# Kernel tuning notes

Measured on AMD Instinct MI355X. Metric: run time of the kernel, lower is better.

The kernel has to match this reference:

```python
import jax, jax.numpy as jnp
import numpy as np

K_NN = 3  # knn(feat_y, feat_x, 3, ...) in the original

def setup_inputs() -> dict:
    key = jax.random.key(0)
    k1, k2, k3, k4, k5, k6 = jax.random.split(key, 6)
    B, C, H, W = 2, 64, 112, 112
    S, G = 50, 120
    img1_feature = jax.random.normal(k1, (B, C, H, W), dtype=jnp.float32)
    img2_feature = jax.random.normal(k2, (B, C, H, W), dtype=jnp.float32)
    mask1 = jax.random.randint(k3, (B, H, W), 0, 2).astype(bool)
    mask2 = jax.random.randint(k4, (B, H, W), 0, 2).astype(bool)
    src_pixel_group = jax.random.uniform(k5, (B, S, G, 2), dtype=jnp.float32)
    slic = jax.random.randint(k6, (B, H, W), 0, 50).astype(jnp.int32)
    return {"img1_feature": img1_feature, "img2_feature": img2_feature,
            "mask1": mask1, "mask2": mask2,
            "src_pixel_group": src_pixel_group, "slic": slic}

def _form_pred_corr(img1_feature, img2_feature, mask1, mask2):
    B, C, H, W = img1_feature.shape
    N = H * W
    fx = img1_feature.reshape(B, C, N)  # src features  [B,C,N]
    fy = img2_feature.reshape(B, C, N)  # dst features  [B,C,N]
    # cosine-KNN search (no_grad in the original): mask invalid dst pixels
    fxn = fx / (jnp.linalg.norm(fx, axis=1, keepdims=True) + 1e-12)
    fyn = fy / (jnp.linalg.norm(fy, axis=1, keepdims=True) + 1e-12)
    sims = jnp.einsum('bcn,bcm->bnm', fxn, fyn)  # [B,N,M] cosine sim
    sims = jnp.where(mask2.reshape(B, 1, N), sims, -jnp.inf)
    _, idx = jax.lax.top_k(jax.lax.stop_gradient(sims), K_NN)  # [B,N,K]
    # gather raw dst features at the K matched pixels: [B,N,K,C]
    fyT = fy.transpose(0, 2, 1)  # [B,M,C]
    gath = jax.vmap(lambda f, i: f[i])(fyT, idx.reshape(B, -1)).reshape(B, N, K_NN, C)
    # weights = raw dot product feat_x . feat_y (matches sim_xy in source)
    w = jnp.einsum('bnkc,bnc->bnk', gath, fx.transpose(0, 2, 1))  # [B,N,K]
    hh = (idx // W).astype(w.dtype)  # dst row coords
    ww = (idx % W).astype(w.dtype)   # dst col coords
    den = jnp.sum(w, axis=2)  # [B,N]
    num = jnp.stack([jnp.sum(hh * w, axis=2), jnp.sum(ww * w, axis=2)], axis=-1)
    pred = num / den[..., None]  # weighted-average dst position [B,N,2]
    pred_corr = jnp.where(mask1[..., None], pred.reshape(B, H, W, 2), -1.0)
    return pred_corr

def _slic_gather(pred_corr, src_pixel_group, norm_h):
    B, H, W, _ = pred_corr.shape
    S, G = src_pixel_group.shape[1], src_pixel_group.shape[2]
    # round(src * H), clamp to [0, H-1] (256/255 in the original at H=256)
    pix = jnp.clip(jnp.round(src_pixel_group * H).astype(jnp.int32), 0, H - 1)
    lin = pix[..., 0] * W + pix[..., 1]  # [B,S,G]
    pcf = pred_corr.reshape(B, H * W, 2)
    dst = jax.vmap(lambda p, l: p[l])(pcf, lin.reshape(B, S * G))
    return dst.reshape(B, S, G, 2) / norm_h

def reference(img1_feature, img2_feature, mask1, mask2, src_pixel_group, slic):
    pred_corr = _form_pred_corr(img1_feature, img2_feature, mask1, mask2)
    dst_pixel_group = _slic_gather(pred_corr, src_pixel_group, slic.shape[1])
    return pred_corr, dst_pixel_group
```

## Files before the change

kernel.cpp:

```cpp
#include <hip/hip_runtime.h>
#include <math.h>

typedef _Float16 f16;
typedef f16 f16x8 __attribute__((ext_vector_type(8)));
typedef float f32x16 __attribute__((ext_vector_type(16)));
typedef unsigned short u16;
typedef unsigned int u32;
typedef unsigned long long u64;
typedef u32 u32x4 __attribute__((ext_vector_type(4)));

#define B_ 2
#define C_ 64
#define KS 5
#define H_ 112
#define W_ 112
#define N_ 12544
#define S_ 50
#define G_ 120
#define SPLIT 8
#define LCAP 4
#define CPR (SPLIT*2*LCAP)
#define TMAX 400
#define CMAPN 12800
#define CH 13

#define NEGINF (-__builtin_inff())
#define FMED3 __builtin_amdgcn_fmed3f

union U16B { uint4 u; f16x8 h; f16 e[8]; };


__global__ void detect_fmt(const u32* __restrict__ m1, const u32* __restrict__ m2,
                           int nw, int* __restrict__ hdr) {
    __shared__ u32 s[2];
    if (threadIdx.x == 0) { s[0] = 0; s[1] = 0; }
    __syncthreads();
    u32 a = 0, bb = 0;
    for (int i = threadIdx.x; i < nw; i += blockDim.x) {
        a  |= m1[i] & 0xFFFFFF00u;
        bb |= m2[i] & 0xFFFFFF00u;
    }
    if (a)  atomicOr(&s[0], 1u);
    if (bb) atomicOr(&s[1], 1u);
    __syncthreads();
    if (threadIdx.x == 0) { hdr[0] = s[0] ? 1 : 0; hdr[1] = s[1] ? 1 : 0; }
}

__global__ __launch_bounds__(1024)
void scan_compact(const unsigned char* __restrict__ m1,
                  const unsigned char* __restrict__ m2,
                  int* __restrict__ hdr,
                  int* __restrict__ slotX, int* __restrict__ slotY,
                  int* __restrict__ cmapX, int* __restrict__ cmapY) {
    const int side = blockIdx.x >> 1;
    const int b = blockIdx.x & 1;
    const unsigned char* mk = side ? m2 : m1;
    const int flag = hdr[side];
    int* slotmap = side ? slotY : slotX;
    int* cmap    = side ? cmapY : cmapX;
    const int cntidx = side ? (2 + b) : (4 + b);

    __shared__ int ssum[1024];
    const int tid = threadIdx.x;
    const int m0 = tid * CH;

    u32 vbits = 0; int cnt = 0;
    #pragma unroll
    for (int i = 0; i < CH; ++i) {
        int m = m0 + i;
        int v = 0;
        if (m < N_) {
            int t = b * N_ + m;
            v = flag ? (mk[t] != 0) : (((const int*)mk)[t] != 0);
        }
        vbits |= (u32)v << i;
        cnt += v;
    }
    ssum[tid] = cnt;
    __syncthreads();
    #pragma unroll
    for (int d = 1; d < 1024; d <<= 1) {
        int v = (tid >= d) ? ssum[tid - d] : 0;
        __syncthreads();
        ssum[tid] += v;
        __syncthreads();
    }
    int slot = ssum[tid] - cnt;
    #pragma unroll
    for (int i = 0; i < CH; ++i) {
        int m = m0 + i;
        if (m < N_) {
            int t = b * N_ + m;
            if ((vbits >> i) & 1) {
                slotmap[t] = slot;
                cmap[b * CMAPN + slot] = m;
                slot++;
            } else slotmap[t] = -1;
        }
    }
    if (tid == 1023) hdr[cntidx] = ssum[1023];
}

__global__ void prep(const float* __restrict__ fx, const float* __restrict__ fy,
                     const unsigned char* __restrict__ mask2b,
                     const int* __restrict__ hdr,
                     const int* __restrict__ slotX, const int* __restrict__ slotY,
                     f16* __restrict__ fxq, float* __restrict__ fxT,
                     float* __restrict__ fynT, f16* __restrict__ fynq,
                     float* __restrict__ nyeps, float* __restrict__ minf,
                     float* __restrict__ out) {
    int t = blockIdx.x * blockDim.x + threadIdx.x;
    if (t >= B_ * N_) return;
    int b = t / N_;

    if (blockIdx.y == 0) {
        const float* src = fx + (size_t)b * C_ * N_ + (t - b * N_);
        float v[64];
        #pragma unroll
        for (int c = 0; c < C_; ++c) v[c] = src[(size_t)c * N_];

        float4* xT = (float4*)(fxT + (size_t)t * C_);
        #pragma unroll
        for (int c4 = 0; c4 < 16; ++c4)
            xT[c4] = make_float4(v[c4*4], v[c4*4+1], v[c4*4+2], v[c4*4+3]);

        int slot = slotX[t];
        if (slot < 0) {
            out[2 * (size_t)t] = -1.0f;
            out[2 * (size_t)t + 1] = -1.0f;
            return;
        }
        int tile = slot >> 5, r = slot & 31;
        uint4* q4 = (uint4*)fxq;
        size_t cb = (size_t)(b * TMAX + tile) * (KS * 64);
        #pragma unroll
        for (int ks = 0; ks < KS; ++ks) {
            #pragma unroll
            for (int hi = 0; hi < 2; ++hi) {
                U16B tmp;
                #pragma unroll
                for (int i = 0; i < 8; ++i) {
                    int k = 16 * ks + 8 * hi + i;
                    float val = (k < 64) ? v[k] : ((k == 64) ? 1.0f : 0.0f);
                    tmp.e[i] = (f16)val;
                }
                q4[cb + (size_t)ks * 64 + hi * 32 + r] = tmp.u;
            }
        }
    } else {
        const float* src = fy + (size_t)b * C_ * N_ + (t - b * N_);
        float v[64];
        float ss = 0.f;
        #pragma unroll
        for (int c = 0; c < C_; ++c) { v[c] = src[(size_t)c * N_]; ss = fmaf(v[c], v[c], ss); }
        float ny = sqrtf(ss) + 1e-12f;
        nyeps[t] = ny;
        int slot = slotY[t];
        minf[t] = (slot >= 0) ? 0.0f : NEGINF;

        float* dT = fynT + (size_t)t * C_;
        #pragma unroll
        for (int c = 0; c < C_; ++c) dT[c] = v[c] / ny;

        if (slot < 0) return;
        int tile = slot >> 5, r = slot & 31;
        uint4* q4 = (uint4*)fynq;
        size_t cb = (size_t)(b * TMAX + tile) * (KS * 64);
        #pragma unroll
        for (int ks = 0; ks < KS; ++ks) {
            #pragma unroll
            for (int hi = 0; hi < 2; ++hi) {
                U16B tmp;
                #pragma unroll
                for (int i = 0; i < 8; ++i) {
                    int k = 16 * ks + 8 * hi + i;
                    float val = (k < 64) ? (v[k] / ny) : ((k == 64) ? 128.0f : 0.0f);
                    tmp.e[i] = (f16)val;
                }
                q4[cb + (size_t)ks * 64 + hi * 32 + r] = tmp.u;
            }
        }
    }
}

__global__ void padfill(int* __restrict__ hdr, uint4* __restrict__ fynq4,
                        uint4* __restrict__ fxq4, int* __restrict__ cmapY,
                        int* __restrict__ cmapX) {
    int tid = threadIdx.x;
    __shared__ int sMY[2], sNX[2], sCY[2], sCX[2];
    if (tid == 0) {
        for (int b = 0; b < B_; ++b) {
            int cy = hdr[2 + b], cx = hdr[4 + b];
            int my = (cy + 255) & ~255;
            int nx = (cx + 63) & ~63;
            hdr[6 + b] = my; hdr[8 + b] = nx;
            sMY[b] = my; sNX[b] = nx; sCY[b] = cy; sCX[b] = cx;
        }
    }
    __syncthreads();
    uint4 z = make_uint4(0, 0, 0, 0);
    for (int b = 0; b < B_; ++b) {
        for (int p = sCY[b] + tid; p < sMY[b]; p += blockDim.x) {
            cmapY[b * CMAPN + p] = 0;
            int tile = p >> 5, r = p & 31;
            size_t cb = (size_t)(b * TMAX + tile) * (KS * 64);
            #pragma unroll
            for (int ks = 0; ks < KS; ++ks) {
                fynq4[cb + (size_t)ks * 64 + r] = z;
                fynq4[cb + (size_t)ks * 64 + 32 + r] = z;
            }
        }
        for (int p = sCX[b] + tid; p < sNX[b]; p += blockDim.x) {
            cmapX[b * CMAPN + p] = 0;
            int tile = p >> 5, r = p & 31;
            size_t cb = (size_t)(b * TMAX + tile) * (KS * 64);
            #pragma unroll
            for (int ks = 0; ks < KS; ++ks) {
                fxq4[cb + (size_t)ks * 64 + r] = z;
                fxq4[cb + (size_t)ks * 64 + 32 + r] = z;
            }
        }
    }
}

#define LDA(dst, t) { _Pragma("unroll") \
    for (int ks = 0; ks < KS; ++ks) \
        dst[ks] = fyb8[((size_t)(t) * KS + ks) * 64]; }

#define MFMAC(acc, a) { \
    acc = __builtin_amdgcn_mfma_f32_32x32x16_f16(a[0], bfr[0], zvec, 0, 0, 0); \
    acc = __builtin_amdgcn_mfma_f32_32x32x16_f16(a[1], bfr[1], acc, 0, 0, 0); \
    acc = __builtin_amdgcn_mfma_f32_32x32x16_f16(a[2], bfr[2], acc, 0, 0, 0); \
    acc = __builtin_amdgcn_mfma_f32_32x32x16_f16(a[3], bfr[3], acc, 0, 0, 0); \
    acc = __builtin_amdgcn_mfma_f32_32x32x16_f16(a[4], bfr[4], acc, 0, 0, 0); }

#define EXTRACT(acc, bse) { \
    _Pragma("unroll") \
    for (int r = 0; r < 16; ++r) { \
        u32 pb_ = (__float_as_uint(acc[r]) & VMASK) | ((bse) + (u32)r); \
        float p_ = __uint_as_float(pb_); \
        b4 = FMED3(p_, b3, b4); \
        b3 = FMED3(p_, b2, b3); \
        b2 = FMED3(p_, b1, b2); \
        b1 = fmaxf(p_, b1); } }

#define CELL(a, t) { f32x16 acc_; MFMAC(acc_, a); EXTRACT(acc_, (u32)((t) * 16)); }

__global__ __launch_bounds__(128, 4)
void stage1(const f16* __restrict__ fxq, const f16* __restrict__ fynq,
            const int* __restrict__ hdr,
            u32* __restrict__ cvals, u16* __restrict__ cidx) {
    const int tid = threadIdx.x;
    const int lane = tid & 63, w = tid >> 6;
    const int lo = lane & 31, hi = lane >> 5;
    const int gid = blockIdx.x;
    const int panel = gid & 15;
    const int b = panel >> 3, split = panel & 7;
    const int nt = (gid >> 4) * 2 + w;
    const int NXb = hdr[8 + b];
    if (nt * 32 >= NXb) return;
    const int TPSr = hdr[6 + b] >> 8;
    const int tbase = split * TPSr;

    const f16x8* fxq8 = (const f16x8*)fxq;
    const f16x8* fyb8 = (const f16x8*)fynq + ((size_t)(b * TMAX + tbase) * KS) * 64 + lane;

    u32 VMASK;
    asm("v_mov_b32 %0, 0xFFFFFC00" : "=v"(VMASK));

    f16x8 bfr[KS];
    #pragma unroll
    for (int ks = 0; ks < KS; ++ks)
        bfr[ks] = fxq8[((size_t)((b * TMAX + nt) * KS + ks)) * 64 + lane];

    f32x16 zvec = {};
    float b1 = 0.f, b2 = 0.f, b3 = 0.f, b4 = 0.f;

    f16x8 aA[KS], aB[KS];
    LDA(aA, 0);
    int t = 0;
    #pragma unroll 1
    for (; t + 1 < TPSr; t += 2) {
        LDA(aB, t + 1);
        CELL(aA, t);
        if (t + 2 < TPSr) LDA(aA, t + 2);
        CELL(aB, t + 1);
    }
    if (t < TPSr) CELL(aA, t);

    int n = nt * 32 + lo;
    size_t base = (((size_t)(b * N_ + n) * SPLIT + split) * 2 + hi) * LCAP;
    u32 pb0 = __float_as_uint(b1), pb1 = __float_as_uint(b2);
    u32 pb2 = __float_as_uint(b3), pb3 = __float_as_uint(b4);
    u32x4 pv = {pb0, pb1, pb2, pb3};
    u64 pidx = 0;
    u32 pbs[4] = {pb0, pb1, pb2, pb3};
    #pragma unroll
    for (int k = 0; k < 4; ++k) {
        int idx10 = (int)(pbs[k] & 1023u);
        int tl = idx10 >> 4, r = idx10 & 15;
        u32 mc = (u32)((tbase + tl) * 32 + (r & 3) + ((r >> 2) << 3) + (hi << 2));
        pidx |= (u64)(mc & 0xFFFFu) << (16 * k);
    }
    __builtin_nontemporal_store(pv, (u32x4*)&cvals[base]);
    __builtin_nontemporal_store(pidx, (u64*)&cidx[base]);
}

__global__ __launch_bounds__(256)
void rescore(const u32* __restrict__ cvals, const u16* __restrict__ cidx,
             const float* __restrict__ fxT, const float* __restrict__ fynT,
             const float* __restrict__ nyeps, const float* __restrict__ minf,
             const int* __restrict__ cmapX, const int* __restrict__ cmapY,
             const int* __restrict__ hdr, float* __restrict__ out) {
    int gwf = blockIdx.x * 4 + (threadIdx.x >> 6);
    int lane = threadIdx.x & 63;
    int b = gwf / N_, slot = gwf - b * N_;
    if (slot >= hdr[4 + b]) return;
    int orig_n = cmapX[b * CMAPN + slot];

    float vn = __uint_as_float(cvals[(size_t)(b * N_ + slot) * CPR + lane]);
    int cm = cidx[(size_t)(b * N_ + slot) * CPR + lane];

    float cur = vn;
    float t3 = NEGINF;
    #pragma unroll
    for (int r = 0; r < 3; ++r) {
        float c = cur;
        #pragma unroll
        for (int off = 32; off >= 1; off >>= 1) c = fmaxf(c, __shfl_xor(c, off));
        t3 = c;
        cur = (cur == c) ? NEGINF : cur;
    }
    bool redo = (vn >= t3 - 0.125f);

    float rnk = NEGINF, wgt = 0.f;
    int midx = 0x7fffffff;
    if (redo) {
        int om = cmapY[b * CMAPN + cm];
        const float4* xq4 = (const float4*)(fxT + ((size_t)b * N_ + orig_n) * C_);
        const float4* fr4 = (const float4*)(fynT + ((size_t)b * N_ + om) * C_);
        float a = 0.f;
        #pragma unroll
        for (int c4 = 0; c4 < 16; ++c4) {
            float4 xf = xq4[c4];
            float4 f  = fr4[c4];
            a = fmaf(xf.x, f.x, a);
            a = fmaf(xf.y, f.y, a);
            a = fmaf(xf.z, f.z, a);
            a = fmaf(xf.w, f.w, a);
        }
        rnk = a + minf[(size_t)b * N_ + om];
        wgt = a * nyeps[(size_t)b * N_ + om];
        midx = om;
    }

    int wi[3]; float ww[3];
    #pragma unroll
    for (int r = 0; r < 3; ++r) {
        float cv = rnk; int ci = midx; float cw = wgt;
        #pragma unroll
        for (int off = 32; off >= 1; off >>= 1) {
            float ov = __shfl_xor(cv, off);
            int   oi = __shfl_xor(ci, off);
            float ow = __shfl_xor(cw, off);
            bool take = (ov > cv) || (ov == cv && oi < ci);
            cv = take ? ov : cv; ci = take ? oi : ci; cw = take ? ow : cw;
        }
        wi[r] = ci; ww[r] = cw;
        if (midx == ci) rnk = NEGINF;
    }

    if (lane == 0) {
        float w0 = ww[0], w1 = ww[1], w2 = ww[2];
        float h0 = (float)(wi[0] / W_), h1 = (float)(wi[1] / W_), h2 = (float)(wi[2] / W_);
        float q0 = (float)(wi[0] % W_), q1 = (float)(wi[1] % W_), q2 = (float)(wi[2] % W_);
        float den = w0 + w1 + w2;
        float ph = (h0 * w0 + h1 * w1 + h2 * w2) / den;
        float pw = (q0 * w0 + q1 * w1 + q2 * w2) / den;
        out[2 * ((size_t)b * N_ + orig_n)]     = ph;
        out[2 * ((size_t)b * N_ + orig_n) + 1] = pw;
    }
}

__global__ void slic_gather(const float* __restrict__ spg,
                            const float* __restrict__ pred,
                            float* __restrict__ outg) {
    int t = blockIdx.x * blockDim.x + threadIdx.x;
    if (t >= B_ * S_ * G_) return;
    int b = t / (S_ * G_);
    float vh = spg[2 * t], vw = spg[2 * t + 1];
    int ph = (int)rintf(vh * (float)H_);
    int pw = (int)rintf(vw * (float)H_);
    ph = ph < 0 ? 0 : (ph > H_ - 1 ? H_ - 1 : ph);
    pw = pw < 0 ? 0 : (pw > H_ - 1 ? H_ - 1 : pw);
    int lin = ph * W_ + pw;
    outg[2 * t]     = pred[((size_t)b * N_ + lin) * 2]     / (float)H_;
    outg[2 * t + 1] = pred[((size_t)b * N_ + lin) * 2 + 1] / (float)H_;
}

extern "C" void kernel_launch(void* const* d_in, const int* in_sizes, int n_in,
                              void* d_out, int out_size, void* d_ws, size_t ws_size,
                              hipStream_t stream) {
    const float* img1 = (const float*)d_in[0];
    const float* img2 = (const float*)d_in[1];
    const void*  mask1 = d_in[2];
    const void*  mask2 = d_in[3];
    const float* spg = (const float*)d_in[4];
    float* out = (float*)d_out;

    char* ws = (char*)d_ws;
    size_t off = 0;
    int*   hdr   = (int*)(ws + off);            off += 256;
    float* fynT  = (float*)(ws + off);          off += (size_t)B_ * N_ * C_ * 4;
    float* fxT   = (float*)(ws + off);          off += (size_t)B_ * N_ * C_ * 4;
    f16*   fxq   = (f16*)(ws + off);            off += (size_t)B_ * TMAX * KS * 64 * 16;
    f16*   fynq  = (f16*)(ws + off);            off += (size_t)B_ * TMAX * KS * 64 * 16;
    float* nyeps = (float*)(ws + off);          off += (size_t)B_ * N_ * 4;
    float* minf  = (float*)(ws + off);          off += (size_t)B_ * N_ * 4;
    int*   cmapY = (int*)(ws + off);            off += (size_t)B_ * CMAPN * 4;
    int*   cmapX = (int*)(ws + off);            off += (size_t)B_ * CMAPN * 4;
    int*   slotX = (int*)(ws + off);            off += (size_t)B_ * N_ * 4;
    int*   slotY = (int*)(ws + off);            off += (size_t)B_ * N_ * 4;
    u32*   cvals = (u32*)(ws + off);            off += (size_t)B_ * N_ * CPR * 4;
    u16*   cidx  = (u16*)(ws + off);            off += (size_t)B_ * N_ * CPR * 2;

    detect_fmt<<<1, 1024, 0, stream>>>((const u32*)mask1, (const u32*)mask2,
                                       (B_ * N_) / 4, hdr);
    scan_compact<<<4, 1024, 0, stream>>>((const unsigned char*)mask1,
                                         (const unsigned char*)mask2, hdr,
                                         slotX, slotY, cmapX, cmapY);
    dim3 gp((B_ * N_) / 256, 2);
    prep<<<gp, 256, 0, stream>>>(img1, img2, (const unsigned char*)mask2, hdr,
                                 slotX, slotY, fxq, fxT, fynT, fynq,
                                 nyeps, minf, out);
    padfill<<<1, 512, 0, stream>>>(hdr, (uint4*)fynq, (uint4*)fxq, cmapY, cmapX);

    stage1<<<3200, 128, 0, stream>>>(fxq, fynq, hdr, cvals, cidx);

    rescore<<<(B_ * N_) / 4, 256, 0, stream>>>(
        cvals, cidx, fxT, fynT, nyeps, minf, cmapX, cmapY, hdr, out);

    slic_gather<<<(B_ * S_ * G_ + 255) / 256, 256, 0, stream>>>(
        spg, out, out + (size_t)B_ * N_ * 2);
}
```

Measured before the change: 92.80 us.

## Fold mask format detection into scan and replace padfill with upfront zerofill

Removes the single-block detect_fmt kernel by having each scan_compact block detect the mask byte format itself, and replaces the serial single-block padfill with a wide grid-stride zerofill launched first. stage1 now computes padded counts from hdr directly. prep caches normalized dst features to avoid recomputing divisions. The aim is to cut small serial kernels from the critical path, at the cost of zeroing the full quantized buffers each call instead of only the pad region.

```diff
diff --git a/kernel.cpp b/kernel.cpp
--- a/kernel.cpp
+++ b/kernel.cpp
@@ -30,20 +30,15 @@
 union U16B { uint4 u; f16x8 h; f16 e[8]; };
 
 
-__global__ void detect_fmt(const u32* __restrict__ m1, const u32* __restrict__ m2,
-                           int nw, int* __restrict__ hdr) {
-    __shared__ u32 s[2];
-    if (threadIdx.x == 0) { s[0] = 0; s[1] = 0; }
-    __syncthreads();
-    u32 a = 0, bb = 0;
-    for (int i = threadIdx.x; i < nw; i += blockDim.x) {
-        a  |= m1[i] & 0xFFFFFF00u;
-        bb |= m2[i] & 0xFFFFFF00u;
-    }
-    if (a)  atomicOr(&s[0], 1u);
-    if (bb) atomicOr(&s[1], 1u);
-    __syncthreads();
-    if (threadIdx.x == 0) { hdr[0] = s[0] ? 1 : 0; hdr[1] = s[1] ? 1 : 0; }
+__global__ void zerofill(uint4* __restrict__ fxq4, uint4* __restrict__ fynq4,
+                         int* __restrict__ cmapX, int* __restrict__ cmapY) {
+    int i = blockIdx.x * blockDim.x + threadIdx.x;
+    int stride = gridDim.x * blockDim.x;
+    uint4 z = make_uint4(0, 0, 0, 0);
+    const int NQ = B_ * TMAX * KS * 64;
+    for (int k = i; k < NQ; k += stride) { fxq4[k] = z; fynq4[k] = z; }
+    const int NC = B_ * CMAPN;
+    for (int k = i; k < NC; k += stride) { cmapX[k] = 0; cmapY[k] = 0; }
 }
 
 __global__ __launch_bounds__(1024)
@@ -55,15 +50,23 @@
     const int side = blockIdx.x >> 1;
     const int b = blockIdx.x & 1;
     const unsigned char* mk = side ? m2 : m1;
-    const int flag = hdr[side];
     int* slotmap = side ? slotY : slotX;
     int* cmap    = side ? cmapY : cmapX;
     const int cntidx = side ? (2 + b) : (4 + b);
-
+    const int tid = threadIdx.x;
+
+    __shared__ int sflag;
     __shared__ int ssum[1024];
-    const int tid = threadIdx.x;
+    if (tid == 0) sflag = 0;
+    __syncthreads();
+    const u32* mw = (const u32*)mk;
+    u32 acc = 0;
+    for (int i = tid; i < (B_ * N_) / 4; i += 1024) acc |= mw[i] & 0xFFFFFF00u;
+    if (acc) atomicOr(&sflag, 1);
+    __syncthreads();
+    const int flag = sflag;
+
     const int m0 = tid * CH;
-
     u32 vbits = 0; int cnt = 0;
     #pragma unroll
     for (int i = 0; i < CH; ++i) {
@@ -102,8 +105,6 @@
 }
 
 __global__ void prep(const float* __restrict__ fx, const float* __restrict__ fy,
-                     const unsigned char* __restrict__ mask2b,
-                     const int* __restrict__ hdr,
                      const int* __restrict__ slotX, const int* __restrict__ slotY,
                      f16* __restrict__ fxq, float* __restrict__ fxT,
                      float* __restrict__ fynT, f16* __restrict__ fynq,
@@ -149,7 +150,7 @@
         }
     } else {
         const float* src = fy + (size_t)b * C_ * N_ + (t - b * N_);
-        float v[64];
+        float v[64], dv[64];
         float ss = 0.f;
         #pragma unroll
         for (int c = 0; c < C_; ++c) { v[c] = src[(size_t)c * N_]; ss = fmaf(v[c], v[c], ss); }
@@ -160,7 +161,7 @@
 
         float* dT = fynT + (size_t)t * C_;
         #pragma unroll
-        for (int c = 0; c < C_; ++c) dT[c] = v[c] / ny;
+        for (int c = 0; c < C_; ++c) { dv[c] = v[c] / ny; dT[c] = dv[c]; }
 
         if (slot < 0) return;
         int tile = slot >> 5, r = slot & 31;
@@ -174,50 +175,10 @@
                 #pragma unroll
                 for (int i = 0; i < 8; ++i) {
                     int k = 16 * ks + 8 * hi + i;
-                    float val = (k < 64) ? (v[k] / ny) : ((k == 64) ? 128.0f : 0.0f);
+                    float val = (k < 64) ? dv[k] : ((k == 64) ? 128.0f : 0.0f);
                     tmp.e[i] = (f16)val;
                 }
                 q4[cb + (size_t)ks * 64 + hi * 32 + r] = tmp.u;
-            }
-        }
-    }
-}
-
-__global__ void padfill(int* __restrict__ hdr, uint4* __restrict__ fynq4,
-                        uint4* __restrict__ fxq4, int* __restrict__ cmapY,
-                        int* __restrict__ cmapX) {
-    int tid = threadIdx.x;
-    __shared__ int sMY[2], sNX[2], sCY[2], sCX[2];
-    if (tid == 0) {
-        for (int b = 0; b < B_; ++b) {
-            int cy = hdr[2 + b], cx = hdr[4 + b];
-            int my = (cy + 255) & ~255;
-            int nx = (cx + 63) & ~63;
-            hdr[6 + b] = my; hdr[8 + b] = nx;
-            sMY[b] = my; sNX[b] = nx; sCY[b] = cy; sCX[b] = cx;
-        }
-    }
-    __syncthreads();
-    uint4 z = make_uint4(0, 0, 0, 0);
-    for (int b = 0; b < B_; ++b) {
-        for (int p = sCY[b] + tid; p < sMY[b]; p += blockDim.x) {
-            cmapY[b * CMAPN + p] = 0;
-            int tile = p >> 5, r = p & 31;
-            size_t cb = (size_t)(b * TMAX + tile) * (KS * 64);
-            #pragma unroll
-            for (int ks = 0; ks < KS; ++ks) {
-                fynq4[cb + (size_t)ks * 64 + r] = z;
-                fynq4[cb + (size_t)ks * 64 + 32 + r] = z;
-            }
-        }
-        for (int p = sCX[b] + tid; p < sNX[b]; p += blockDim.x) {
-            cmapX[b * CMAPN + p] = 0;
-            int tile = p >> 5, r = p & 31;
-            size_t cb = (size_t)(b * TMAX + tile) * (KS * 64);
-            #pragma unroll
-            for (int ks = 0; ks < KS; ++ks) {
-                fxq4[cb + (size_t)ks * 64 + r] = z;
-                fxq4[cb + (size_t)ks * 64 + 32 + r] = z;
             }
         }
     }
@@ -257,9 +218,9 @@
     const int panel = gid & 15;
     const int b = panel >> 3, split = panel & 7;
     const int nt = (gid >> 4) * 2 + w;
-    const int NXb = hdr[8 + b];
+    const int NXb = (hdr[4 + b] + 63) & ~63;
     if (nt * 32 >= NXb) return;
-    const int TPSr = hdr[6 + b] >> 8;
+    const int TPSr = ((hdr[2 + b] + 255) & ~255) >> 8;
     const int tbase = split * TPSr;
 
     const f16x8* fxq8 = (const f16x8*)fxq;
@@ -424,16 +385,13 @@
     u32*   cvals = (u32*)(ws + off);            off += (size_t)B_ * N_ * CPR * 4;
     u16*   cidx  = (u16*)(ws + off);            off += (size_t)B_ * N_ * CPR * 2;
 
-    detect_fmt<<<1, 1024, 0, stream>>>((const u32*)mask1, (const u32*)mask2,
-                                       (B_ * N_) / 4, hdr);
+    zerofill<<<1024, 256, 0, stream>>>((uint4*)fxq, (uint4*)fynq, cmapX, cmapY);
     scan_compact<<<4, 1024, 0, stream>>>((const unsigned char*)mask1,
                                          (const unsigned char*)mask2, hdr,
                                          slotX, slotY, cmapX, cmapY);
     dim3 gp((B_ * N_) / 256, 2);
-    prep<<<gp, 256, 0, stream>>>(img1, img2, (const unsigned char*)mask2, hdr,
-                                 slotX, slotY, fxq, fxT, fynT, fynq,
-                                 nyeps, minf, out);
-    padfill<<<1, 512, 0, stream>>>(hdr, (uint4*)fynq, (uint4*)fxq, cmapY, cmapX);
+    prep<<<gp, 256, 0, stream>>>(img1, img2, slotX, slotY,
+                                 fxq, fxT, fynT, fynq, nyeps, minf, out);
 
     stage1<<<3200, 128, 0, stream>>>(fxq, fynq, hdr, cvals, cidx);
 
```

Result: faster. 88.64 us (-4.5%).
